# Performance work log

Measured on AMD Instinct MI355X. Metric: run time of the kernel, lower is better.

Reference implementation:

```python
import jax, jax.numpy as jnp
import numpy as np

# dims
B, S, D, H, L = 4, 2048, 512, 8, 4
DH = D // H          # head dim 64
MLP = 2048
VOCAB = 32000
BLK = 128            # block size
NB = S // BLK        # 16 blocks
SINK_ITERS = 8       # sinkhorn normalization iterations
NEG = -1e9


def _sinusoid_pos_emb(max_len, d):
    pos = np.arange(max_len, dtype=np.float32)[:, None]
    div = np.exp(np.arange(0, d, 2, dtype=np.float32) * (-np.log(10000.0) / d))
    pe = np.zeros((max_len, d), np.float32)
    pe[:, 0::2] = np.sin(pos * div)
    pe[:, 1::2] = np.cos(pos * div)
    return pe

_PE = jnp.asarray(_sinusoid_pos_emb(S, D))


def setup_inputs() -> dict:
    key = jax.random.key(0)
    ks = jax.random.split(key, 12)
    g = lambda k, shape, s=0.02: jax.random.normal(k, shape, jnp.float32) * s
    tokens = jax.random.randint(ks[0], (B, S), 0, VOCAB)
    return {
        "tokens": tokens,
        "embed": g(ks[1], (VOCAB, D), 1.0),
        "ln1_s": jnp.ones((L, D)), "ln1_b": jnp.zeros((L, D)),
        "wq": g(ks[2], (L, D, H, DH)),
        "wk": g(ks[3], (L, D, H, DH)),
        "wv": g(ks[4], (L, D, H, DH)),
        "wo": g(ks[5], (L, H, DH, D)),
        "sort_w": g(ks[6], (L, H, DH, NB)),
        "ln2_s": jnp.ones((L, D)), "ln2_b": jnp.zeros((L, D)),
        "w1": g(ks[7], (L, D, MLP)), "b1": jnp.zeros((L, MLP)),
        "w2": g(ks[8], (L, MLP, D)), "b2": jnp.zeros((L, D)),
        "lnf_s": jnp.ones((D,)), "lnf_b": jnp.zeros((D,)),
    }


def _ln(x, s, b):
    m = jnp.mean(x, axis=-1, keepdims=True)
    v = jnp.mean(jnp.square(x - m), axis=-1, keepdims=True)
    return (x - m) * jax.lax.rsqrt(v + 1e-6) * s + b


def _sinkhorn(log_alpha):
    # iterative row/col normalization in log space -> soft permutation
    for _ in range(SINK_ITERS):
        log_alpha = log_alpha - jax.nn.logsumexp(log_alpha, axis=-1, keepdims=True)
        log_alpha = log_alpha - jax.nn.logsumexp(log_alpha, axis=-2, keepdims=True)
    return jnp.exp(log_alpha)


def _forward(tokens, embed, ln1_s, ln1_b, wq, wk, wv, wo, sort_w,
             ln2_s, ln2_b, w1, b1, w2, b2, lnf_s, lnf_b):
    pad = (tokens > 0)                       # [B,S] key padding mask
    mb = pad.reshape(B, NB, BLK).astype(jnp.float32)  # block mask
    x = embed[tokens] + _PE[None, :S]        # [B,S,D]
    scale = 1.0 / jnp.sqrt(jnp.float32(DH))
    for l in range(L):
        h = _ln(x, ln1_s[l], ln1_b[l])
        q = jnp.einsum('bsd,dhf->bshf', h, wq[l]) * scale
        k = jnp.einsum('bsd,dhf->bshf', h, wk[l])
        v = jnp.einsum('bsd,dhf->bshf', h, wv[l])
        qb = q.reshape(B, NB, BLK, H, DH)
        kb = k.reshape(B, NB, BLK, H, DH)
        vb = v.reshape(B, NB, BLK, H, DH)
        # sort net: block summary of keys -> block-to-block logits per head
        ksum = kb.sum(axis=2)                               # [B,NB,H,DH]
        logits = jnp.einsum('bnhd,hdm->bhnm', ksum, sort_w[l])
        perm = _sinkhorn(logits)                            # [B,H,NB,NB]
        sk = jnp.einsum('bhnm,bmchd->bnchd', perm, kb)      # sorted key blocks
        sv = jnp.einsum('bhnm,bmchd->bnchd', perm, vb)
        kcat = jnp.concatenate([kb, sk], axis=2)            # [B,NB,2BLK,H,DH]
        vcat = jnp.concatenate([vb, sv], axis=2)
        scores = jnp.einsum('bnqhd,bnkhd->bhnqk', qb, kcat)  # [B,H,NB,BLK,2BLK]
        # padding bias: local part from block mask, sorted part via permuted mask
        local = jnp.broadcast_to(mb[:, None, :, None, :], (B, H, NB, 1, BLK))
        smask = (jnp.einsum('bhnm,bmc->bhnc', jax.lax.stop_gradient(perm), mb) > 0.5)
        smask = smask[:, :, :, None, :].astype(jnp.float32)
        full_mask = jnp.concatenate([local, jnp.broadcast_to(smask, (B, H, NB, 1, BLK))], axis=-1)
        scores = scores + jnp.where(full_mask > 0.5, 0.0, NEG)
        attn = jax.nn.softmax(scores, axis=-1)
        o = jnp.einsum('bhnqk,bnkhd->bnqhd', attn, vcat).reshape(B, S, H, DH)
        x = x + jnp.einsum('bshd,hdD->bsD', o, wo[l])
        y = _ln(x, ln2_s[l], ln2_b[l])
        y = jax.nn.gelu(jnp.einsum('bsd,df->bsf', y, w1[l]) + b1[l])
        x = x + jnp.einsum('bsf,fd->bsd', y, w2[l]) + b2[l]
    return _ln(x, lnf_s, lnf_b)


def reference(tokens, embed, ln1_s, ln1_b, wq, wk, wv, wo, sort_w,
              ln2_s, ln2_b, w1, b1, w2, b2, lnf_s, lnf_b):
    return _forward(tokens, embed, ln1_s, ln1_b, wq, wk, wv, wo, sort_w,
                    ln2_s, ln2_b, w1, b1, w2, b2, lnf_s, lnf_b)
```

## Files before the change

kernel.cpp:

```cpp
#include <hip/hip_runtime.h>
#include <math.h>

#define B_ 4
#define S_ 2048
#define D_ 512
#define H_ 8
#define L_ 4
#define DH_ 64
#define MLP_ 2048
#define BLK_ 128
#define NB_ 16
#define NEGINF -1e9f
#define NXE ((size_t)B_ * S_ * D_)

typedef unsigned short u16;
typedef __attribute__((ext_vector_type(8))) short short8;
typedef __attribute__((ext_vector_type(4))) short short4v;
typedef __attribute__((ext_vector_type(4))) float f32x4;

__device__ __forceinline__ float bf2f(u16 s) {
  return __uint_as_float(((unsigned)s) << 16);
}
__device__ __forceinline__ u16 f2bf(float f) {
  unsigned u = __float_as_uint(f);
  unsigned r = (u + 0x7FFFu + ((u >> 16) & 1u)) >> 16;
  return (u16)r;
}

__device__ __forceinline__ void gll16(const void* g, void* l) {
  __builtin_amdgcn_global_load_lds(
      (const __attribute__((address_space(1))) unsigned int*)g,
      (__attribute__((address_space(3))) unsigned int*)l, 16, 0, 0);
}

__global__ __launch_bounds__(128) void k_embed(const int* __restrict__ tokens,
                                               const float* __restrict__ embed,
                                               float* __restrict__ x) {
  int s = blockIdx.x;
  int tid = threadIdx.x;
  const float c = -logf(10000.0f) / (float)D_;
  int d = tid * 4;
  float pe[4];
#pragma unroll
  for (int j = 0; j < 4; ++j) {
    int dd = d + j;
    int i2 = dd >> 1;
    float freq = __expf(c * (float)(2 * i2));
    float ang = (float)s * freq;
    pe[j] = (dd & 1) ? cosf(ang) : sinf(ang);
  }
#pragma unroll
  for (int b = 0; b < B_; ++b) {
    int tok = tokens[b * S_ + s];
    float4 e = *(const float4*)(embed + (size_t)tok * D_ + d);
    *(float4*)(x + (size_t)(b * S_ + s) * D_ + d) =
        make_float4(e.x + pe[0], e.y + pe[1], e.z + pe[2], e.w + pe[3]);
  }
}

template <typename OT>
__global__ __launch_bounds__(256) void k_ln(const float* __restrict__ x,
                                            const float* __restrict__ sc,
                                            const float* __restrict__ bi,
                                            OT* __restrict__ out, int rows) {
  int row = blockIdx.x * 4 + (threadIdx.x >> 6);
  int lane = threadIdx.x & 63;
  if (row >= rows) return;
  const float* xr = x + (size_t)row * D_;
  float v[8];
  float4 a = *(const float4*)(xr + lane * 8);
  float4 b = *(const float4*)(xr + lane * 8 + 4);
  v[0]=a.x; v[1]=a.y; v[2]=a.z; v[3]=a.w; v[4]=b.x; v[5]=b.y; v[6]=b.z; v[7]=b.w;
  float sum = 0.f;
#pragma unroll
  for (int j = 0; j < 8; ++j) sum += v[j];
#pragma unroll
  for (int off = 32; off; off >>= 1) sum += __shfl_xor(sum, off);
  float mean = sum * (1.0f / D_);
  float var = 0.f;
#pragma unroll
  for (int j = 0; j < 8; ++j) { float d = v[j] - mean; var += d * d; }
#pragma unroll
  for (int off = 32; off; off >>= 1) var += __shfl_xor(var, off);
  float rstd = rsqrtf(var * (1.0f / D_) + 1e-6f);
  float o[8];
#pragma unroll
  for (int j = 0; j < 8; ++j) {
    int d = lane * 8 + j;
    o[j] = (v[j] - mean) * rstd * sc[d] + bi[d];
  }
  if constexpr (sizeof(OT) == 4) {
    float* op = (float*)out + (size_t)row * D_ + lane * 8;
    *(float4*)op = make_float4(o[0], o[1], o[2], o[3]);
    *(float4*)(op + 4) = make_float4(o[4], o[5], o[6], o[7]);
  } else {
    u16* op = (u16*)out + (size_t)row * D_ + lane * 8;
    short8 o8;
#pragma unroll
    for (int j = 0; j < 8; ++j) o8[j] = (short)f2bf(o[j]);
    *(short8*)op = o8;
  }
}

__global__ __launch_bounds__(256) void k_transp(const float* __restrict__ W,
                                                u16* __restrict__ WT, int K, int N,
                                                size_t wStrideZ, size_t tStrideZ) {
  __shared__ float t[32][33];
  const float* Wl = W + (size_t)blockIdx.z * wStrideZ;
  u16* WTl = WT + (size_t)blockIdx.z * tStrideZ;
  int k0 = blockIdx.x * 32, n0 = blockIdx.y * 32;
  int x = threadIdx.x & 31, y = threadIdx.x >> 5;
#pragma unroll
  for (int yy = y; yy < 32; yy += 8)
    t[yy][x] = Wl[(size_t)(k0 + yy) * N + n0 + x];
  __syncthreads();
#pragma unroll
  for (int yy = y; yy < 32; yy += 8)
    WTl[(size_t)(n0 + yy) * K + k0 + x] = f2bf(t[x][yy]);
}

__device__ __forceinline__ float gelu_f(float x) {
  float y = 0.7978845608028654f * (x + 0.044715f * x * x * x);
  float e = __expf(2.0f * y);
  return x - x / (e + 1.0f);
}

enum { EPI_STORE = 0, EPI_ADD = 1, EPI_GELU = 2, EPI_ADDBIAS = 3, EPI_QKV = 4 };

template <int EPI>
__device__ __forceinline__ void epilogue_elem(u16* Cb, float* Cf, float bv,
                                              int row, int col, int N, float alpha,
                                              float v) {
  if (EPI == EPI_STORE) {
    Cb[(size_t)row * N + col] = f2bf(v * alpha);
  } else if (EPI == EPI_QKV) {
    u16* dst = Cb + (size_t)(col >> 9) * NXE;
    float al = (col < 512) ? alpha : 1.0f;
    dst[(size_t)row * D_ + (col & 511)] = f2bf(v * al);
  } else if (EPI == EPI_GELU) {
    Cb[(size_t)row * N + col] = f2bf(gelu_f(v + bv));
  } else if (EPI == EPI_ADD) {
    Cf[(size_t)row * N + col] += v;
  } else {
    Cf[(size_t)row * N + col] += v + bv;
  }
}

template <int EPI>
__global__ __launch_bounds__(256) void k_mm64(const u16* __restrict__ A,
                                              const u16* __restrict__ BT,
                                              const float* __restrict__ bias,
                                              u16* __restrict__ Cb,
                                              float* __restrict__ Cf,
                                              int M, int N, int K, float alpha) {
  __shared__ u16 Al[2][64 * 64];
  __shared__ u16 Bl[2][64 * 64];
  int tid = threadIdx.x;
  int lane = tid & 63;
  int wave = tid >> 6;
  int nwg = gridDim.x * gridDim.y;
  int bid = blockIdx.y * gridDim.x + blockIdx.x;
  int cpx = nwg >> 3;
  int swz = (bid & 7) * cpx + (bid >> 3);
  int bx = swz % gridDim.x, by = swz / gridDim.x;
  int m0 = by * 64, n0 = bx * 64;
  int wm = (wave >> 1) * 32, wn = (wave & 1) * 32;
  int l15 = lane & 15, l4 = lane >> 4;

  int row0 = tid >> 3;
  int lchunk = (tid & 7) ^ (row0 & 7);
  const u16* Ag0 = A + (size_t)(m0 + row0) * K + lchunk * 8;
  const u16* Ag1 = Ag0 + (size_t)32 * K;
  const u16* Bg0 = BT + (size_t)(n0 + row0) * K + lchunk * 8;
  const u16* Bg1 = Bg0 + (size_t)32 * K;

  auto stage = [&](int buf, int kt) {
    int k0 = kt * 64;
    char* AlB = (char*)(&Al[buf][0]) + (wave * 64) * 16;
    char* BlB = (char*)(&Bl[buf][0]) + (wave * 64) * 16;
    gll16(Ag0 + k0, AlB);
    gll16(Ag1 + k0, AlB + 256 * 16);
    gll16(Bg0 + k0, BlB);
    gll16(Bg1 + k0, BlB + 256 * 16);
  };

  f32x4 zero = {0.f, 0.f, 0.f, 0.f};
  f32x4 acc[2][2];
#pragma unroll
  for (int i = 0; i < 2; ++i)
#pragma unroll
    for (int j = 0; j < 2; ++j) acc[i][j] = zero;

  int NK = K >> 6;
  stage(0, 0);
  asm volatile("s_waitcnt vmcnt(0)" ::: "memory");
  __syncthreads();

  for (int t = 0; t < NK; ++t) {
    if (t + 1 < NK) stage((t + 1) & 1, t + 1);
    const u16* Ab = &Al[t & 1][0];
    const u16* Bb = &Bl[t & 1][0];
    short8 af[2][2], bf4[2][2];
#pragma unroll
    for (int i = 0; i < 2; ++i) {
      int ar = wm + i * 16 + l15;
#pragma unroll
      for (int ks = 0; ks < 2; ++ks)
        af[i][ks] = *(const short8*)(Ab + ar * 64 + (((ks * 4 + l4) ^ (ar & 7))) * 8);
    }
#pragma unroll
    for (int j = 0; j < 2; ++j) {
      int br = wn + j * 16 + l15;
#pragma unroll
      for (int ks = 0; ks < 2; ++ks)
        bf4[j][ks] = *(const short8*)(Bb + br * 64 + (((ks * 4 + l4) ^ (br & 7))) * 8);
    }
#pragma unroll
    for (int ks = 0; ks < 2; ++ks)
#pragma unroll
      for (int i = 0; i < 2; ++i)
#pragma unroll
        for (int j = 0; j < 2; ++j)
          acc[i][j] = __builtin_amdgcn_mfma_f32_16x16x32_bf16(af[i][ks], bf4[j][ks], acc[i][j], 0, 0, 0);
    asm volatile("s_waitcnt vmcnt(0)" ::: "memory");
    __syncthreads();
  }

#pragma unroll
  for (int i = 0; i < 2; ++i)
#pragma unroll
    for (int j = 0; j < 2; ++j) {
      int col = n0 + wn + j * 16 + l15;
      float bv = (EPI == EPI_GELU || EPI == EPI_ADDBIAS) ? bias[col] : 0.f;
#pragma unroll
      for (int r = 0; r < 4; ++r) {
        int row = m0 + wm + i * 16 + l4 * 4 + r;
        epilogue_elem<EPI>(Cb, Cf, bv, row, col, N, alpha, acc[i][j][r]);
      }
    }
}

__global__ __launch_bounds__(256) void k_sort(const u16* __restrict__ K,
                                              const float* __restrict__ sortw_l,
                                              const int* __restrict__ tokens,
                                              float* __restrict__ PM,
                                              float* __restrict__ SM) {
  int bh = blockIdx.x;
  int h = bh & (H_ - 1), b = bh >> 3;
  int tid = threadIdx.x;
  __shared__ float ks[NB_][DH_];
  __shared__ float mbm[NB_][BLK_];
  __shared__ float buf[256];
  __shared__ float red[16];

  for (int it = tid; it < S_; it += 256)
    mbm[it >> 7][it & 127] = (tokens[b * S_ + it] > 0) ? 1.f : 0.f;

  if (tid < 128) {
    int n = tid >> 3, ch = (tid & 7) * 8;
    const u16* kp = K + (((size_t)(b * S_ + n * BLK_) * H_) + h) * DH_ + ch;
    float s[8] = {};
    for (int c = 0; c < BLK_; ++c) {
      short8 v = *(const short8*)(kp + (size_t)c * (H_ * DH_));
#pragma unroll
      for (int j = 0; j < 8; ++j) s[j] += bf2f((u16)v[j]);
    }
#pragma unroll
    for (int j = 0; j < 8; ++j) ks[n][ch + j] = s[j];
  }
  __syncthreads();

  int n = tid >> 4, m = tid & 15;
  const float* wp = sortw_l + (size_t)h * DH_ * NB_;
  float la = 0.f;
#pragma unroll
  for (int d = 0; d < DH_; ++d) la += ks[n][d] * wp[d * NB_ + m];

  for (int it = 0; it < 8; ++it) {
    buf[tid] = la;
    __syncthreads();
    if (m == 0) {
      float mx = buf[n * 16];
      for (int t = 1; t < 16; ++t) mx = fmaxf(mx, buf[n * 16 + t]);
      float s = 0.f;
      for (int t = 0; t < 16; ++t) s += __expf(buf[n * 16 + t] - mx);
      red[n] = mx + __logf(s);
    }
    __syncthreads();
    la -= red[n];
    buf[tid] = la;
    __syncthreads();
    if (tid < 16) {
      float mx = buf[tid];
      for (int t = 1; t < 16; ++t) mx = fmaxf(mx, buf[t * 16 + tid]);
      float s = 0.f;
      for (int t = 0; t < 16; ++t) s += __expf(buf[t * 16 + tid] - mx);
      red[tid] = mx + __logf(s);
    }
    __syncthreads();
    la -= red[m];
    __syncthreads();
  }
  float pm = __expf(la);
  PM[(size_t)bh * 256 + tid] = pm;
  buf[tid] = pm;
  __syncthreads();

  for (int it = tid; it < NB_ * BLK_; it += 256) {
    int nn = it >> 7, c = it & 127;
    float s = 0.f;
#pragma unroll
    for (int mm = 0; mm < NB_; ++mm) s += buf[nn * 16 + mm] * mbm[mm][c];
    SM[(size_t)bh * (NB_ * BLK_) + it] = s;
  }
}

__global__ __launch_bounds__(512) void k_attn(
    const u16* __restrict__ Q, const u16* __restrict__ Kg, const u16* __restrict__ Vg,
    const float* __restrict__ PMg, const int* __restrict__ tokens,
    const float* __restrict__ smask, u16* __restrict__ O) {
  int n = blockIdx.x, h = blockIdx.y, b = blockIdx.z;
  int tid = threadIdx.x;
  int lane = tid & 63;
  int w = tid >> 6;
  int l15 = lane & 15, l4 = lane >> 4;

  __shared__ u16 KV[16384];
  __shared__ u16 Pl[32768];
  __shared__ float sbias[256];
  __shared__ float prs[NB_];

#pragma unroll
  for (int s = 0; s < 2; ++s) {
    int c = s * 512 + tid;
    int r = c >> 3;
    int fs = (c & 7) ^ (r & 7);
    gll16(Kg + (((size_t)(b * S_ + n * BLK_ + r) * H_) + h) * DH_ + fs * 8,
          (char*)KV + (s * 512 + w * 64) * 16);
  }

  short8 qf0, qf1;
  {
    const u16* qp = Q + (((size_t)(b * S_ + n * BLK_ + w * 16 + l15) * H_) + h) * DH_ + l4 * 8;
    qf0 = *(const short8*)(qp);
    qf1 = *(const short8*)(qp + 32);
  }

  int vr = tid >> 2, vq = (tid & 3) * 16;
  short8 vloc[2];
  {
    const u16* vbase = Vg + (((size_t)(b * S_ + n * BLK_ + vr) * H_) + h) * DH_ + vq;
    vloc[0] = *(const short8*)(vbase);
    vloc[1] = *(const short8*)(vbase + 8);
  }

  if (tid < NB_) prs[tid] = PMg[(((size_t)(b * H_ + h) * NB_) + n) * NB_ + tid];
  if (tid < 256) {
    float mval = (tid < BLK_)
        ? ((tokens[b * S_ + n * BLK_ + tid] > 0) ? 1.f : 0.f)
        : smask[(((size_t)(b * H_ + h) * NB_) + n) * BLK_ + (tid - BLK_)];
    sbias[tid] = (mval > 0.5f) ? 0.f : NEGINF;
  }
  __syncthreads();

#pragma unroll
  for (int s = 0; s < 2; ++s) {
    int c = 1024 + s * 512 + tid;
    int r = c >> 3;
    int rs = r & 127;
    int p = c & 7;
    int ls = p ^ (r & 7);
    const u16* kp = Kg + (((size_t)(b * S_ + rs) * H_) + h) * DH_ + ls * 8;
    float ak[8] = {};
#pragma unroll
    for (int m = 0; m < NB_; ++m) {
      float pr = prs[m];
      short8 kv = *(const short8*)(kp + (size_t)m * (BLK_ * H_ * DH_));
#pragma unroll
      for (int j = 0; j < 8; ++j) ak[j] += pr * bf2f((u16)kv[j]);
    }
    short8 ok;
#pragma unroll
    for (int j = 0; j < 8; ++j) ok[j] = (short)f2bf(ak[j]);
    *(short8*)(KV + r * 64 + p * 8) = ok;
  }

  short8 vsrt[2];
  {
    const u16* vp = Vg + (((size_t)(b * S_ + vr) * H_) + h) * DH_ + vq;
    float av[16] = {};
#pragma unroll
    for (int m = 0; m < NB_; ++m) {
      float pr = prs[m];
      const u16* vm = vp + (size_t)m * (BLK_ * H_ * DH_);
      short8 v0 = *(const short8*)(vm);
      short8 v1 = *(const short8*)(vm + 8);
#pragma unroll
      for (int j = 0; j < 8; ++j) {
        av[j] += pr * bf2f((u16)v0[j]);
        av[8 + j] += pr * bf2f((u16)v1[j]);
      }
    }
#pragma unroll
    for (int j = 0; j < 8; ++j) {
      vsrt[0][j] = (short)f2bf(av[j]);
      vsrt[1][j] = (short)f2bf(av[8 + j]);
    }
  }
  __syncthreads();

  f32x4 zero = {0.f, 0.f, 0.f, 0.f};
  f32x4 st[16];
#pragma unroll
  for (int m = 0; m < 16; ++m) st[m] = zero;
#pragma unroll
  for (int m = 0; m < 16; ++m) {
    int arow = m * 16 + l15;
    const u16* kb = KV + arow * 64;
    int sw = arow & 7;
    short8 a0 = *(const short8*)(kb + ((l4 ^ sw) * 8));
    short8 a1 = *(const short8*)(kb + (((4 + l4) ^ sw) * 8));
    st[m] = __builtin_amdgcn_mfma_f32_16x16x32_bf16(a0, qf0, st[m], 0, 0, 0);
    st[m] = __builtin_amdgcn_mfma_f32_16x16x32_bf16(a1, qf1, st[m], 0, 0, 0);
  }

  float mx = -3.0e38f;
#pragma unroll
  for (int m = 0; m < 16; ++m)
#pragma unroll
    for (int r = 0; r < 4; ++r) {
      st[m][r] += sbias[m * 16 + l4 * 4 + r];
      mx = fmaxf(mx, st[m][r]);
    }
  mx = fmaxf(mx, __shfl_xor(mx, 16));
  mx = fmaxf(mx, __shfl_xor(mx, 32));
  float sum = 0.f;
#pragma unroll
  for (int m = 0; m < 16; ++m)
#pragma unroll
    for (int r = 0; r < 4; ++r) {
      float e = __expf(st[m][r] - mx);
      st[m][r] = e;
      sum += e;
    }
  sum += __shfl_xor(sum, 16);
  sum += __shfl_xor(sum, 32);
  float inv = 1.0f / sum;

  int q = w * 16 + l15;
  int qx = q & 31;
#pragma unroll
  for (int m = 0; m < 16; ++m) {
    short4v p4;
#pragma unroll
    for (int r = 0; r < 4; ++r) p4[r] = (short)f2bf(st[m][r] * inv);
    int slot = (m * 4 + l4) ^ qx;
    *(short4v*)(Pl + q * 256 + slot * 4) = p4;
  }
  __syncthreads();

#pragma unroll
  for (int half = 0; half < 2; ++half)
#pragma unroll
    for (int j = 0; j < 8; ++j) {
      int d = vq + half * 8 + j;
      KV[d * 256 + (((vr >> 3) ^ (d & 7)) * 8) + (vr & 7)] = (u16)vloc[half][j];
    }
  {
    int r2 = vr + 128;
#pragma unroll
    for (int half = 0; half < 2; ++half)
#pragma unroll
      for (int j = 0; j < 8; ++j) {
        int d = vq + half * 8 + j;
        KV[d * 256 + (((r2 >> 3) ^ (d & 7)) * 8) + (r2 & 7)] = (u16)vsrt[half][j];
      }
  }
  __syncthreads();

  f32x4 oacc[4];
#pragma unroll
  for (int nf = 0; nf < 4; ++nf) oacc[nf] = zero;
#pragma unroll
  for (int kk = 0; kk < 8; ++kk) {
    int s0 = (kk * 8 + l4 * 2) ^ qx;
    int s1 = (kk * 8 + l4 * 2 + 1) ^ qx;
    short4v a0 = *(const short4v*)(Pl + q * 256 + s0 * 4);
    short4v a1 = *(const short4v*)(Pl + q * 256 + s1 * 4);
    short8 af;
#pragma unroll
    for (int j = 0; j < 4; ++j) { af[j] = a0[j]; af[4 + j] = a1[j]; }
#pragma unroll
    for (int nf = 0; nf < 4; ++nf) {
      int d = nf * 16 + l15;
      short8 bf = *(const short8*)(KV + d * 256 + (((kk * 4 + l4) ^ (d & 7)) * 8));
      oacc[nf] = __builtin_amdgcn_mfma_f32_16x16x32_bf16(af, bf, oacc[nf], 0, 0, 0);
    }
  }

  u16* ob = O + (((size_t)(b * S_ + n * BLK_) * H_) + h) * DH_;
#pragma unroll
  for (int nf = 0; nf < 4; ++nf) {
    int d = nf * 16 + l15;
#pragma unroll
    for (int r = 0; r < 4; ++r) {
      int qq = w * 16 + l4 * 4 + r;
      ob[(size_t)qq * (H_ * DH_) + d] = f2bf(oacc[nf][r]);
    }
  }
}

extern "C" void kernel_launch(void* const* d_in, const int* in_sizes, int n_in,
                              void* d_out, int out_size, void* d_ws, size_t ws_size,
                              hipStream_t stream) {
  const int* tokens = (const int*)d_in[0];
  const float* embed = (const float*)d_in[1];
  const float* ln1_s = (const float*)d_in[2];
  const float* ln1_b = (const float*)d_in[3];
  const float* wq = (const float*)d_in[4];
  const float* wk = (const float*)d_in[5];
  const float* wv = (const float*)d_in[6];
  const float* wo = (const float*)d_in[7];
  const float* sortw = (const float*)d_in[8];
  const float* ln2_s = (const float*)d_in[9];
  const float* ln2_b = (const float*)d_in[10];
  const float* w1 = (const float*)d_in[11];
  const float* b1 = (const float*)d_in[12];
  const float* w2 = (const float*)d_in[13];
  const float* b2 = (const float*)d_in[14];
  const float* lnf_s = (const float*)d_in[15];
  const float* lnf_b = (const float*)d_in[16];
  float* out = (float*)d_out;

  const size_t NX = NXE;
  float* ws = (float*)d_ws;
  float* X = ws;
  float* ATT = ws + NX;
  u16* HID = (u16*)ATT;
  u16* Hbf = (u16*)(ws + 5 * NX);
  u16* Qb = Hbf + NX;
  u16* Kb = Qb + NX;
  u16* Vb = Kb + NX;
  u16* Ob = Hbf;
  float* PM = (float*)(Vb + NX);
  float* SM = PM + (size_t)B_ * H_ * NB_ * NB_;
  u16* WT = (u16*)(SM + (size_t)B_ * H_ * NB_ * BLK_);
  u16* wqkvT = WT;
  u16* woT = wqkvT + (size_t)L_ * 3 * D_ * D_;
  u16* w1T = woT + (size_t)L_ * D_ * D_;
  u16* w2T = w1T + (size_t)L_ * D_ * MLP_;

  const int rows = B_ * S_;
  const float scale = 0.125f;
  const size_t qkvStride = (size_t)3 * D_ * D_;

  k_transp<<<dim3(16, 16, L_), 256, 0, stream>>>(wq, wqkvT, D_, D_, (size_t)D_ * D_, qkvStride);
  k_transp<<<dim3(16, 16, L_), 256, 0, stream>>>(wk, wqkvT + (size_t)512 * 512, D_, D_, (size_t)D_ * D_, qkvStride);
  k_transp<<<dim3(16, 16, L_), 256, 0, stream>>>(wv, wqkvT + (size_t)1024 * 512, D_, D_, (size_t)D_ * D_, qkvStride);
  k_transp<<<dim3(16, 16, L_), 256, 0, stream>>>(wo, woT, D_, D_, (size_t)D_ * D_, (size_t)D_ * D_);
  k_transp<<<dim3(16, 64, L_), 256, 0, stream>>>(w1, w1T, D_, MLP_, (size_t)D_ * MLP_, (size_t)MLP_ * D_);
  k_transp<<<dim3(64, 16, L_), 256, 0, stream>>>(w2, w2T, MLP_, D_, (size_t)MLP_ * D_, (size_t)D_ * MLP_);

  k_embed<<<S_, 128, 0, stream>>>(tokens, embed, X);

  for (int l = 0; l < L_; ++l) {
    k_ln<u16><<<rows / 4, 256, 0, stream>>>(X, ln1_s + l * D_, ln1_b + l * D_, Hbf, rows);
    dim3 gqkv(1536 / 64, rows / 64);
    k_mm64<EPI_QKV><<<gqkv, 256, 0, stream>>>(Hbf, wqkvT + (size_t)l * qkvStride, nullptr, Qb, nullptr, rows, 1536, D_, scale);
    k_sort<<<B_ * H_, 256, 0, stream>>>(Kb, sortw + (size_t)l * H_ * DH_ * NB_, tokens, PM, SM);
    dim3 gatt(NB_, H_, B_);
    k_attn<<<gatt, 512, 0, stream>>>(Qb, Kb, Vb, PM, tokens, SM, Ob);
    dim3 go(D_ / 64, rows / 64);
    k_mm64<EPI_ADD><<<go, 256, 0, stream>>>(Ob, woT + (size_t)l * D_ * D_, nullptr, nullptr, X, rows, D_, D_, 1.0f);
    k_ln<u16><<<rows / 4, 256, 0, stream>>>(X, ln2_s + l * D_, ln2_b + l * D_, Hbf, rows);
    dim3 g2(MLP_ / 64, rows / 64);
    k_mm64<EPI_GELU><<<g2, 256, 0, stream>>>(Hbf, w1T + (size_t)l * D_ * MLP_, b1 + (size_t)l * MLP_, HID, nullptr, rows, MLP_, D_, 1.0f);
    dim3 g3(D_ / 64, rows / 64);
    k_mm64<EPI_ADDBIAS><<<g3, 256, 0, stream>>>(HID, w2T + (size_t)l * MLP_ * D_, b2 + (size_t)l * D_, nullptr, X, rows, D_, MLP_, 1.0f);
  }
  k_ln<float><<<rows / 4, 256, 0, stream>>>(X, lnf_s, lnf_b, out, rows);
}
```

Measured before the change: 737.9 us.

## Add 128x128-tile GEMM for MLP up-projection and precompute LDS offsets

Adds a new k_mm kernel with 128x128 output tiles, 32-wide K steps and 4x4 MFMA accumulators per wave, and uses it for the GELU up-projection GEMM in place of the 64x64 kernel. This raises the arithmetic intensity per loaded LDS tile and reduces global traffic. The 64x64 kernel and the attention QK loop now precompute swizzled LDS offsets and advance pointers instead of recomputing indices, and the K loop is unrolled by two with fixed double-buffer pointers. The larger tile launches fewer workgroups (256 for this shape) and uses more registers, which could lower occupancy. The unroll-by-two loop assumes the number of K steps is even.

Result: no change. 746.8 us (+1.2%).

```diff
diff --git a/kernel.cpp b/kernel.cpp
--- a/kernel.cpp
+++ b/kernel.cpp
@@ -144,6 +144,100 @@
   } else {
     Cf[(size_t)row * N + col] += v + bv;
   }
+}
+
+template <int EPI>
+__global__ __launch_bounds__(256) void k_mm(const u16* __restrict__ A,
+                                            const u16* __restrict__ BT,
+                                            const float* __restrict__ bias,
+                                            u16* __restrict__ Cb,
+                                            float* __restrict__ Cf,
+                                            int M, int N, int K, float alpha) {
+  __shared__ u16 Al[2][128 * 32];
+  __shared__ u16 Bl[2][128 * 32];
+  int tid = threadIdx.x;
+  int lane = tid & 63;
+  int wave = tid >> 6;
+  int nwg = gridDim.x * gridDim.y;
+  int bid = blockIdx.y * gridDim.x + blockIdx.x;
+  int cpx = nwg >> 3;
+  int swz = (bid & 7) * cpx + (bid >> 3);
+  int bx = swz % gridDim.x, by = swz / gridDim.x;
+  int m0 = by * 128, n0 = bx * 128;
+  int wm = (wave >> 1) * 64, wn = (wave & 1) * 64;
+  int l15 = lane & 15, l4 = lane >> 4;
+
+  int schunk = (tid & 3) ^ ((tid >> 3) & 3);
+  const u16* pa0 = A + (size_t)(m0 + (tid >> 2)) * K + schunk * 8;
+  const u16* pa1 = pa0 + (size_t)64 * K;
+  const u16* pb0 = BT + (size_t)(n0 + (tid >> 2)) * K + schunk * 8;
+  const u16* pb1 = pb0 + (size_t)64 * K;
+  char* dA0 = (char*)&Al[0][0] + wave * 1024;
+  char* dA1 = (char*)&Al[1][0] + wave * 1024;
+  char* dB0 = (char*)&Bl[0][0] + wave * 1024;
+  char* dB1 = (char*)&Bl[1][0] + wave * 1024;
+
+  auto stage = [&](char* da, char* db) {
+    gll16(pa0, da); gll16(pa1, da + 4096);
+    gll16(pb0, db); gll16(pb1, db + 4096);
+    pa0 += 32; pa1 += 32; pb0 += 32; pb1 += 32;
+  };
+
+  int rchunk = (l4 ^ ((l15 >> 1) & 3)) * 8;
+  int aofs[4], bofs[4];
+#pragma unroll
+  for (int i = 0; i < 4; ++i) aofs[i] = (wm + i * 16 + l15) * 32 + rchunk;
+#pragma unroll
+  for (int j = 0; j < 4; ++j) bofs[j] = (wn + j * 16 + l15) * 32 + rchunk;
+
+  f32x4 zero = {0.f, 0.f, 0.f, 0.f};
+  f32x4 acc[4][4];
+#pragma unroll
+  for (int i = 0; i < 4; ++i)
+#pragma unroll
+    for (int j = 0; j < 4; ++j) acc[i][j] = zero;
+
+  auto compute = [&](const u16* Ab, const u16* Bb) {
+    short8 af[4], bf4[4];
+#pragma unroll
+    for (int i = 0; i < 4; ++i) af[i] = *(const short8*)(Ab + aofs[i]);
+#pragma unroll
+    for (int j = 0; j < 4; ++j) bf4[j] = *(const short8*)(Bb + bofs[j]);
+#pragma unroll
+    for (int i = 0; i < 4; ++i)
+#pragma unroll
+      for (int j = 0; j < 4; ++j)
+        acc[i][j] = __builtin_amdgcn_mfma_f32_16x16x32_bf16(af[i], bf4[j], acc[i][j], 0, 0, 0);
+  };
+
+  int NK = K >> 5;
+  stage(dA0, dB0);
+  asm volatile("s_waitcnt vmcnt(0)" ::: "memory");
+  __syncthreads();
+
+  for (int t = 0; t < NK; t += 2) {
+    stage(dA1, dB1);
+    compute(&Al[0][0], &Bl[0][0]);
+    asm volatile("s_waitcnt vmcnt(0)" ::: "memory");
+    __syncthreads();
+    if (t + 2 < NK) stage(dA0, dB0);
+    compute(&Al[1][0], &Bl[1][0]);
+    asm volatile("s_waitcnt vmcnt(0)" ::: "memory");
+    __syncthreads();
+  }
+
+#pragma unroll
+  for (int i = 0; i < 4; ++i)
+#pragma unroll
+    for (int j = 0; j < 4; ++j) {
+      int col = n0 + wn + j * 16 + l15;
+      float bv = (EPI == EPI_GELU || EPI == EPI_ADDBIAS) ? bias[col] : 0.f;
+#pragma unroll
+      for (int r = 0; r < 4; ++r) {
+        int row = m0 + wm + i * 16 + l4 * 4 + r;
+        epilogue_elem<EPI>(Cb, Cf, bv, row, col, N, alpha, acc[i][j][r]);
+      }
+    }
 }
 
 template <int EPI>
@@ -169,20 +263,30 @@
 
   int row0 = tid >> 3;
   int lchunk = (tid & 7) ^ (row0 & 7);
-  const u16* Ag0 = A + (size_t)(m0 + row0) * K + lchunk * 8;
-  const u16* Ag1 = Ag0 + (size_t)32 * K;
-  const u16* Bg0 = BT + (size_t)(n0 + row0) * K + lchunk * 8;
-  const u16* Bg1 = Bg0 + (size_t)32 * K;
-
-  auto stage = [&](int buf, int kt) {
-    int k0 = kt * 64;
-    char* AlB = (char*)(&Al[buf][0]) + (wave * 64) * 16;
-    char* BlB = (char*)(&Bl[buf][0]) + (wave * 64) * 16;
-    gll16(Ag0 + k0, AlB);
-    gll16(Ag1 + k0, AlB + 256 * 16);
-    gll16(Bg0 + k0, BlB);
-    gll16(Bg1 + k0, BlB + 256 * 16);
+  const u16* pa0 = A + (size_t)(m0 + row0) * K + lchunk * 8;
+  const u16* pa1 = pa0 + (size_t)32 * K;
+  const u16* pb0 = BT + (size_t)(n0 + row0) * K + lchunk * 8;
+  const u16* pb1 = pb0 + (size_t)32 * K;
+  char* dA0 = (char*)&Al[0][0] + wave * 1024;
+  char* dA1 = (char*)&Al[1][0] + wave * 1024;
+  char* dB0 = (char*)&Bl[0][0] + wave * 1024;
+  char* dB1 = (char*)&Bl[1][0] + wave * 1024;
+
+  auto stage = [&](char* da, char* db) {
+    gll16(pa0, da); gll16(pa1, da + 4096);
+    gll16(pb0, db); gll16(pb1, db + 4096);
+    pa0 += 64; pa1 += 64; pb0 += 64; pb1 += 64;
   };
+
+  int swr = l15 & 7;
+  int aofs[2][2], bofs[2][2];
+#pragma unroll
+  for (int i = 0; i < 2; ++i)
+#pragma unroll
+    for (int ks = 0; ks < 2; ++ks) {
+      aofs[i][ks] = (wm + i * 16 + l15) * 64 + (((ks * 4 + l4) ^ swr) * 8);
+      bofs[i][ks] = (wn + i * 16 + l15) * 64 + (((ks * 4 + l4) ^ swr) * 8);
+    }
 
   f32x4 zero = {0.f, 0.f, 0.f, 0.f};
   f32x4 acc[2][2];
@@ -191,30 +295,15 @@
 #pragma unroll
     for (int j = 0; j < 2; ++j) acc[i][j] = zero;
 
-  int NK = K >> 6;
-  stage(0, 0);
-  asm volatile("s_waitcnt vmcnt(0)" ::: "memory");
-  __syncthreads();
-
-  for (int t = 0; t < NK; ++t) {
-    if (t + 1 < NK) stage((t + 1) & 1, t + 1);
-    const u16* Ab = &Al[t & 1][0];
-    const u16* Bb = &Bl[t & 1][0];
+  auto compute = [&](const u16* Ab, const u16* Bb) {
     short8 af[2][2], bf4[2][2];
 #pragma unroll
-    for (int i = 0; i < 2; ++i) {
-      int ar = wm + i * 16 + l15;
-#pragma unroll
-      for (int ks = 0; ks < 2; ++ks)
-        af[i][ks] = *(const short8*)(Ab + ar * 64 + (((ks * 4 + l4) ^ (ar & 7))) * 8);
-    }
-#pragma unroll
-    for (int j = 0; j < 2; ++j) {
-      int br = wn + j * 16 + l15;
-#pragma unroll
-      for (int ks = 0; ks < 2; ++ks)
-        bf4[j][ks] = *(const short8*)(Bb + br * 64 + (((ks * 4 + l4) ^ (br & 7))) * 8);
-    }
+    for (int i = 0; i < 2; ++i)
+#pragma unroll
+      for (int ks = 0; ks < 2; ++ks) {
+        af[i][ks] = *(const short8*)(Ab + aofs[i][ks]);
+        bf4[i][ks] = *(const short8*)(Bb + bofs[i][ks]);
+      }
 #pragma unroll
     for (int ks = 0; ks < 2; ++ks)
 #pragma unroll
@@ -222,6 +311,20 @@
 #pragma unroll
         for (int j = 0; j < 2; ++j)
           acc[i][j] = __builtin_amdgcn_mfma_f32_16x16x32_bf16(af[i][ks], bf4[j][ks], acc[i][j], 0, 0, 0);
+  };
+
+  int NK = K >> 6;
+  stage(dA0, dB0);
+  asm volatile("s_waitcnt vmcnt(0)" ::: "memory");
+  __syncthreads();
+
+  for (int t = 0; t < NK; t += 2) {
+    stage(dA1, dB1);
+    compute(&Al[0][0], &Bl[0][0]);
+    asm volatile("s_waitcnt vmcnt(0)" ::: "memory");
+    __syncthreads();
+    if (t + 2 < NK) stage(dA0, dB0);
+    compute(&Al[1][0], &Bl[1][0]);
     asm volatile("s_waitcnt vmcnt(0)" ::: "memory");
     __syncthreads();
   }
@@ -413,15 +516,17 @@
   f32x4 st[16];
 #pragma unroll
   for (int m = 0; m < 16; ++m) st[m] = zero;
-#pragma unroll
-  for (int m = 0; m < 16; ++m) {
-    int arow = m * 16 + l15;
-    const u16* kb = KV + arow * 64;
-    int sw = arow & 7;
-    short8 a0 = *(const short8*)(kb + ((l4 ^ sw) * 8));
-    short8 a1 = *(const short8*)(kb + (((4 + l4) ^ sw) * 8));
-    st[m] = __builtin_amdgcn_mfma_f32_16x16x32_bf16(a0, qf0, st[m], 0, 0, 0);
-    st[m] = __builtin_amdgcn_mfma_f32_16x16x32_bf16(a1, qf1, st[m], 0, 0, 0);
+  {
+    int swk = l15 & 7;
+    const u16* kb0 = KV + l15 * 64 + ((l4 ^ swk) * 8);
+    const u16* kb1 = KV + l15 * 64 + (((4 + l4) ^ swk) * 8);
+#pragma unroll
+    for (int m = 0; m < 16; ++m) {
+      short8 a0 = *(const short8*)(kb0 + m * 1024);
+      short8 a1 = *(const short8*)(kb1 + m * 1024);
+      st[m] = __builtin_amdgcn_mfma_f32_16x16x32_bf16(a0, qf0, st[m], 0, 0, 0);
+      st[m] = __builtin_amdgcn_mfma_f32_16x16x32_bf16(a1, qf1, st[m], 0, 0, 0);
+    }
   }
 
   float mx = -3.0e38f;
@@ -573,8 +678,8 @@
     dim3 go(D_ / 64, rows / 64);
     k_mm64<EPI_ADD><<<go, 256, 0, stream>>>(Ob, woT + (size_t)l * D_ * D_, nullptr, nullptr, X, rows, D_, D_, 1.0f);
     k_ln<u16><<<rows / 4, 256, 0, stream>>>(X, ln2_s + l * D_, ln2_b + l * D_, Hbf, rows);
-    dim3 g2(MLP_ / 64, rows / 64);
-    k_mm64<EPI_GELU><<<g2, 256, 0, stream>>>(Hbf, w1T + (size_t)l * D_ * MLP_, b1 + (size_t)l * MLP_, HID, nullptr, rows, MLP_, D_, 1.0f);
+    dim3 g2(MLP_ / 128, rows / 128);
+    k_mm<EPI_GELU><<<g2, 256, 0, stream>>>(Hbf, w1T + (size_t)l * D_ * MLP_, b1 + (size_t)l * MLP_, HID, nullptr, rows, MLP_, D_, 1.0f);
     dim3 g3(D_ / 64, rows / 64);
     k_mm64<EPI_ADDBIAS><<<g3, 256, 0, stream>>>(HID, w2T + (size_t)l * MLP_ * D_, b2 + (size_t)l * D_, nullptr, X, rows, D_, MLP_, 1.0f);
   }
```

## Fuse residual add into layernorm, add 128x128 MLP-up GEMM tile

Applied to the files above, without the earlier changes.

The projection and MLP-down GEMMs now store bf16 results to a scratch buffer rather than doing read-modify-write on the fp32 residual. The following layernorm kernel adds that buffer into X and normalizes in a single pass. The MLP-up GEMM moves to a new 128x128-tile kernel with more reuse per workgroup, and the attention K-fragment address math is hoisted out of the loop. The residual branch is now rounded to bf16 before it is added, which costs some precision.

Measured after the change: 727.1 us. No clear change (-1.5%).

```diff
diff --git a/kernel.cpp b/kernel.cpp
--- a/kernel.cpp
+++ b/kernel.cpp
@@ -58,19 +58,27 @@
   }
 }
 
-template <typename OT>
-__global__ __launch_bounds__(256) void k_ln(const float* __restrict__ x,
-                                            const float* __restrict__ sc,
-                                            const float* __restrict__ bi,
-                                            OT* __restrict__ out, int rows) {
+template <typename OT, bool HASY>
+__global__ __launch_bounds__(256) void k_lnadd(float* __restrict__ x,
+                                               const u16* __restrict__ y,
+                                               const float* __restrict__ sc,
+                                               const float* __restrict__ bi,
+                                               OT* __restrict__ out, int rows) {
   int row = blockIdx.x * 4 + (threadIdx.x >> 6);
   int lane = threadIdx.x & 63;
   if (row >= rows) return;
-  const float* xr = x + (size_t)row * D_;
+  float* xr = x + (size_t)row * D_;
   float v[8];
   float4 a = *(const float4*)(xr + lane * 8);
   float4 b = *(const float4*)(xr + lane * 8 + 4);
   v[0]=a.x; v[1]=a.y; v[2]=a.z; v[3]=a.w; v[4]=b.x; v[5]=b.y; v[6]=b.z; v[7]=b.w;
+  if (HASY) {
+    short8 y8 = *(const short8*)(y + (size_t)row * D_ + lane * 8);
+#pragma unroll
+    for (int j = 0; j < 8; ++j) v[j] += bf2f((u16)y8[j]);
+    *(float4*)(xr + lane * 8) = make_float4(v[0], v[1], v[2], v[3]);
+    *(float4*)(xr + lane * 8 + 4) = make_float4(v[4], v[5], v[6], v[7]);
+  }
   float sum = 0.f;
 #pragma unroll
   for (int j = 0; j < 8; ++j) sum += v[j];
@@ -125,10 +133,10 @@
   return x - x / (e + 1.0f);
 }
 
-enum { EPI_STORE = 0, EPI_ADD = 1, EPI_GELU = 2, EPI_ADDBIAS = 3, EPI_QKV = 4 };
+enum { EPI_STORE = 0, EPI_GELU = 2, EPI_QKV = 4, EPI_BSTORE = 5 };
 
 template <int EPI>
-__device__ __forceinline__ void epilogue_elem(u16* Cb, float* Cf, float bv,
+__device__ __forceinline__ void epilogue_elem(u16* Cb, float bv,
                                               int row, int col, int N, float alpha,
                                               float v) {
   if (EPI == EPI_STORE) {
@@ -139,11 +147,93 @@
     dst[(size_t)row * D_ + (col & 511)] = f2bf(v * al);
   } else if (EPI == EPI_GELU) {
     Cb[(size_t)row * N + col] = f2bf(gelu_f(v + bv));
-  } else if (EPI == EPI_ADD) {
-    Cf[(size_t)row * N + col] += v;
-  } else {
-    Cf[(size_t)row * N + col] += v + bv;
-  }
+  } else if (EPI == EPI_BSTORE) {
+    Cb[(size_t)row * N + col] = f2bf(v + bv);
+  }
+}
+
+template <int EPI>
+__global__ __launch_bounds__(256) void k_mm(const u16* __restrict__ A,
+                                            const u16* __restrict__ BT,
+                                            const float* __restrict__ bias,
+                                            u16* __restrict__ Cb,
+                                            int M, int N, int K, float alpha) {
+  __shared__ u16 Al[2][128 * 32];
+  __shared__ u16 Bl[2][128 * 32];
+  int tid = threadIdx.x;
+  int lane = tid & 63;
+  int wave = tid >> 6;
+  int nwg = gridDim.x * gridDim.y;
+  int bid = blockIdx.y * gridDim.x + blockIdx.x;
+  int cpx = nwg >> 3;
+  int swz = (bid & 7) * cpx + (bid >> 3);
+  int bx = swz % gridDim.x, by = swz / gridDim.x;
+  int m0 = by * 128, n0 = bx * 128;
+  int wm = (wave >> 1) * 64, wn = (wave & 1) * 64;
+  int l15 = lane & 15, l4 = lane >> 4;
+
+  int schunk = (tid & 3) ^ ((tid >> 3) & 3);
+  const u16* Ag0 = A + (size_t)(m0 + (tid >> 2)) * K + schunk * 8;
+  const u16* Ag1 = Ag0 + (size_t)64 * K;
+  const u16* Bg0 = BT + (size_t)(n0 + (tid >> 2)) * K + schunk * 8;
+  const u16* Bg1 = Bg0 + (size_t)64 * K;
+
+  auto stage = [&](int buf, int kt) {
+    int k0 = kt * 32;
+    char* AlB = (char*)(&Al[buf][0]) + wave * 1024;
+    char* BlB = (char*)(&Bl[buf][0]) + wave * 1024;
+    gll16(Ag0 + k0, AlB);
+    gll16(Ag1 + k0, AlB + 4096);
+    gll16(Bg0 + k0, BlB);
+    gll16(Bg1 + k0, BlB + 4096);
+  };
+
+  f32x4 zero = {0.f, 0.f, 0.f, 0.f};
+  f32x4 acc[4][4];
+#pragma unroll
+  for (int i = 0; i < 4; ++i)
+#pragma unroll
+    for (int j = 0; j < 4; ++j) acc[i][j] = zero;
+
+  int NK = K >> 5;
+  stage(0, 0);
+  asm volatile("s_waitcnt vmcnt(0)" ::: "memory");
+  __syncthreads();
+
+  int rchunk = (l4 ^ ((l15 >> 1) & 3)) * 8;
+
+  for (int t = 0; t < NK; ++t) {
+    if (t + 1 < NK) stage((t + 1) & 1, t + 1);
+    const u16* Ab = &Al[t & 1][0];
+    const u16* Bb = &Bl[t & 1][0];
+    short8 af[4], bf4[4];
+#pragma unroll
+    for (int i = 0; i < 4; ++i)
+      af[i] = *(const short8*)(Ab + (wm + i * 16 + l15) * 32 + rchunk);
+#pragma unroll
+    for (int j = 0; j < 4; ++j)
+      bf4[j] = *(const short8*)(Bb + (wn + j * 16 + l15) * 32 + rchunk);
+#pragma unroll
+    for (int i = 0; i < 4; ++i)
+#pragma unroll
+      for (int j = 0; j < 4; ++j)
+        acc[i][j] = __builtin_amdgcn_mfma_f32_16x16x32_bf16(af[i], bf4[j], acc[i][j], 0, 0, 0);
+    asm volatile("s_waitcnt vmcnt(0)" ::: "memory");
+    __syncthreads();
+  }
+
+#pragma unroll
+  for (int i = 0; i < 4; ++i)
+#pragma unroll
+    for (int j = 0; j < 4; ++j) {
+      int col = n0 + wn + j * 16 + l15;
+      float bv = (EPI == EPI_GELU || EPI == EPI_BSTORE) ? bias[col] : 0.f;
+#pragma unroll
+      for (int r = 0; r < 4; ++r) {
+        int row = m0 + wm + i * 16 + l4 * 4 + r;
+        epilogue_elem<EPI>(Cb, bv, row, col, N, alpha, acc[i][j][r]);
+      }
+    }
 }
 
 template <int EPI>
@@ -151,7 +241,6 @@
                                               const u16* __restrict__ BT,
                                               const float* __restrict__ bias,
                                               u16* __restrict__ Cb,
-                                              float* __restrict__ Cf,
                                               int M, int N, int K, float alpha) {
   __shared__ u16 Al[2][64 * 64];
   __shared__ u16 Bl[2][64 * 64];
@@ -231,11 +320,11 @@
 #pragma unroll
     for (int j = 0; j < 2; ++j) {
       int col = n0 + wn + j * 16 + l15;
-      float bv = (EPI == EPI_GELU || EPI == EPI_ADDBIAS) ? bias[col] : 0.f;
+      float bv = (EPI == EPI_GELU || EPI == EPI_BSTORE) ? bias[col] : 0.f;
 #pragma unroll
       for (int r = 0; r < 4; ++r) {
         int row = m0 + wm + i * 16 + l4 * 4 + r;
-        epilogue_elem<EPI>(Cb, Cf, bv, row, col, N, alpha, acc[i][j][r]);
+        epilogue_elem<EPI>(Cb, bv, row, col, N, alpha, acc[i][j][r]);
       }
     }
 }
@@ -413,15 +502,17 @@
   f32x4 st[16];
 #pragma unroll
   for (int m = 0; m < 16; ++m) st[m] = zero;
-#pragma unroll
-  for (int m = 0; m < 16; ++m) {
-    int arow = m * 16 + l15;
-    const u16* kb = KV + arow * 64;
-    int sw = arow & 7;
-    short8 a0 = *(const short8*)(kb + ((l4 ^ sw) * 8));
-    short8 a1 = *(const short8*)(kb + (((4 + l4) ^ sw) * 8));
-    st[m] = __builtin_amdgcn_mfma_f32_16x16x32_bf16(a0, qf0, st[m], 0, 0, 0);
-    st[m] = __builtin_amdgcn_mfma_f32_16x16x32_bf16(a1, qf1, st[m], 0, 0, 0);
+  {
+    int swk = l15 & 7;
+    const u16* kb0 = KV + l15 * 64 + ((l4 ^ swk) * 8);
+    const u16* kb1 = KV + l15 * 64 + (((4 + l4) ^ swk) * 8);
+#pragma unroll
+    for (int m = 0; m < 16; ++m) {
+      short8 a0 = *(const short8*)(kb0 + m * 1024);
+      short8 a1 = *(const short8*)(kb1 + m * 1024);
+      st[m] = __builtin_amdgcn_mfma_f32_16x16x32_bf16(a0, qf0, st[m], 0, 0, 0);
+      st[m] = __builtin_amdgcn_mfma_f32_16x16x32_bf16(a1, qf1, st[m], 0, 0, 0);
+    }
   }
 
   float mx = -3.0e38f;
@@ -541,8 +632,9 @@
   u16* Qb = Hbf + NX;
   u16* Kb = Qb + NX;
   u16* Vb = Kb + NX;
+  u16* Yb = Vb + NX;
   u16* Ob = Hbf;
-  float* PM = (float*)(Vb + NX);
+  float* PM = (float*)(Yb + NX);
   float* SM = PM + (size_t)B_ * H_ * NB_ * NB_;
   u16* WT = (u16*)(SM + (size_t)B_ * H_ * NB_ * BLK_);
   u16* wqkvT = WT;
@@ -562,21 +654,24 @@
   k_transp<<<dim3(64, 16, L_), 256, 0, stream>>>(w2, w2T, MLP_, D_, (size_t)MLP_ * D_, (size_t)D_ * MLP_);
 
   k_embed<<<S_, 128, 0, stream>>>(tokens, embed, X);
+  k_lnadd<u16, false><<<rows / 4, 256, 0, stream>>>(X, nullptr, ln1_s, ln1_b, Hbf, rows);
 
   for (int l = 0; l < L_; ++l) {
-    k_ln<u16><<<rows / 4, 256, 0, stream>>>(X, ln1_s + l * D_, ln1_b + l * D_, Hbf, rows);
     dim3 gqkv(1536 / 64, rows / 64);
-    k_mm64<EPI_QKV><<<gqkv, 256, 0, stream>>>(Hbf, wqkvT + (size_t)l * qkvStride, nullptr, Qb, nullptr, rows, 1536, D_, scale);
+    k_mm64<EPI_QKV><<<gqkv, 256, 0, stream>>>(Hbf, wqkvT + (size_t)l * qkvStride, nullptr, Qb, rows, 1536, D_, scale);
     k_sort<<<B_ * H_, 256, 0, stream>>>(Kb, sortw + (size_t)l * H_ * DH_ * NB_, tokens, PM, SM);
     dim3 gatt(NB_, H_, B_);
     k_attn<<<gatt, 512, 0, stream>>>(Qb, Kb, Vb, PM, tokens, SM, Ob);
     dim3 go(D_ / 64, rows / 64);
-    k_mm64<EPI_ADD><<<go, 256, 0, stream>>>(Ob, woT + (size_t)l * D_ * D_, nullptr, nullptr, X, rows, D_, D_, 1.0f);
-    k_ln<u16><<<rows / 4, 256, 0, stream>>>(X, ln2_s + l * D_, ln2_b + l * D_, Hbf, rows);
-    dim3 g2(MLP_ / 64, rows / 64);
-    k_mm64<EPI_GELU><<<g2, 256, 0, stream>>>(Hbf, w1T + (size_t)l * D_ * MLP_, b1 + (size_t)l * MLP_, HID, nullptr, rows, MLP_, D_, 1.0f);
+    k_mm64<EPI_STORE><<<go, 256, 0, stream>>>(Ob, woT + (size_t)l * D_ * D_, nullptr, Yb, rows, D_, D_, 1.0f);
+    k_lnadd<u16, true><<<rows / 4, 256, 0, stream>>>(X, Yb, ln2_s + l * D_, ln2_b + l * D_, Hbf, rows);
+    dim3 g2(MLP_ / 128, rows / 128);
+    k_mm<EPI_GELU><<<g2, 256, 0, stream>>>(Hbf, w1T + (size_t)l * D_ * MLP_, b1 + (size_t)l * MLP_, HID, rows, MLP_, D_, 1.0f);
     dim3 g3(D_ / 64, rows / 64);
-    k_mm64<EPI_ADDBIAS><<<g3, 256, 0, stream>>>(HID, w2T + (size_t)l * MLP_ * D_, b2 + (size_t)l * D_, nullptr, X, rows, D_, MLP_, 1.0f);
-  }
-  k_ln<float><<<rows / 4, 256, 0, stream>>>(X, lnf_s, lnf_b, out, rows);
-}
+    k_mm64<EPI_BSTORE><<<g3, 256, 0, stream>>>(HID, w2T + (size_t)l * MLP_ * D_, b2 + (size_t)l * D_, Yb, rows, D_, MLP_, 1.0f);
+    if (l < L_ - 1) {
+      k_lnadd<u16, true><<<rows / 4, 256, 0, stream>>>(X, Yb, ln1_s + (l + 1) * D_, ln1_b + (l + 1) * D_, Hbf, rows);
+    }
+  }
+  k_lnadd<float, true><<<rows / 4, 256, 0, stream>>>(X, Yb, lnf_s, lnf_b, out, rows);
+}
```
